# Optimization experiments

Hardware: AMD Instinct MI355X
Metric: run time of the kernel (lower is better)

The kernel has to match this reference:

```python
import jax, jax.numpy as jnp
import numpy as np

TAU = 0.5
EPS = 1e-6
RAY_STEPS = 128
N_SECANT = 8
STEPS_IN = 64
STEPS_OUT = 32
RADIUS = 1.0
ADA_START, ADA_END, ADA_DECAY = 2.0, 0.1, 1.5e-5
IT = 100000
DEPTH_NEAR = 0.0
DELTA = float(max(ADA_START * np.exp(-ADA_DECAY * IT), ADA_END))


def _occ_val(p, W1, b1, W2, b2):
    # occupancy probability minus tau (sign change = surface crossing)
    h = jax.nn.softplus(p @ W1 + b1)
    return jax.nn.sigmoid((h @ W2 + b2)[..., 0]) - TAU


def _rgb_alpha(p, v, W1, b1, W2, b2, Wc1, bc1, Wc2, bc2):
    alpha = _occ_val(p, W1, b1, W2, b2) + TAU
    f = jax.nn.relu(jnp.concatenate([p, v], -1) @ Wc1 + bc1)
    rgb = jax.nn.sigmoid(f @ Wc2 + bc2)
    return rgb, alpha


def _forward(pixels, camera_mat, world_mat, scale_mat, W1, b1, W2, b2, Wc1, bc1, Wc2, bc2):
    B, N, _ = pixels.shape
    # transform_to_world with all matrices inverted: p_world = S^-1 W^-1 C^-1 p_hom
    M = jnp.linalg.inv(scale_mat) @ jnp.linalg.inv(world_mat) @ jnp.linalg.inv(camera_mat)
    ones = jnp.ones((B, N, 1), pixels.dtype)
    p_h = jnp.concatenate([pixels, ones, ones], -1)  # (x, y, 1, 1) with depth 1
    pixels_world = jnp.einsum('bij,bnj->bni', M, p_h)[..., :3]
    origin = jnp.array([0.0, 0.0, 0.0, 1.0], pixels.dtype)
    cam0 = jnp.einsum('bij,j->bi', M, origin)[..., :3]                 # (B,3)
    camera_world = jnp.broadcast_to(cam0[:, None, :], (B, N, 3))
    ray = pixels_world - camera_world
    ray = ray / jnp.linalg.norm(ray, axis=-1, keepdims=True)

    # ---- sphere intersection ----
    rcd = jnp.einsum('bnd,bd->bn', ray, cam0)
    under = rcd ** 2 - (jnp.sum(cam0 ** 2, -1)[:, None] - RADIUS ** 2)
    mask_int = under > 0
    s = jnp.sqrt(jnp.where(mask_int, under, 1.0))                      # safe sqrt
    inters = jnp.stack([-s - rcd, s - rcd], -1)
    inters = jnp.where(mask_int[..., None], inters, 0.0)
    inters = jnp.maximum(inters, 0.0)                                  # (B,N,2)
    d_far = inters[..., 1]

    # ---- ray marching + secant root finding (no grad in original) ----
    t = jnp.linspace(0.0, 1.0, RAY_STEPS, dtype=pixels.dtype)
    d_prop = d_far[..., None] * t                                      # (B,N,S)
    p_prop = camera_world[:, :, None, :] + ray[:, :, None, :] * d_prop[..., None]
    val = _occ_val(p_prop, W1, b1, W2, b2)                             # (B,N,S)
    mask_0_free = val[..., 0] < 0
    sign = jnp.sign(val[..., :-1] * val[..., 1:])
    sign = jnp.concatenate([sign, jnp.ones_like(sign[..., :1])], -1)
    cost = sign * jnp.arange(RAY_STEPS, 0, -1, dtype=pixels.dtype)
    ind = jnp.argmin(cost, -1)
    mask_sc = jnp.min(cost, -1) < 0
    f_low = jnp.take_along_axis(val, ind[..., None], -1)[..., 0]
    mask = mask_sc & (f_low < 0) & mask_int & mask_0_free
    ind_hi = jnp.minimum(ind + 1, RAY_STEPS - 1)
    d_low = jnp.take_along_axis(d_prop, ind[..., None], -1)[..., 0]
    d_high = jnp.take_along_axis(d_prop, ind_hi[..., None], -1)[..., 0]
    f_high = jnp.take_along_axis(val, ind_hi[..., None], -1)[..., 0]

    def sec(f_l, f_h, d_l, d_h):
        den = f_h - f_l
        return jnp.where(jnp.abs(den) > 1e-12, -f_l * (d_h - d_l) / den + d_l, 0.5 * (d_l + d_h))

    def body(i, c):
        d_p, d_l, f_l, d_h, f_h = c
        f_m = _occ_val(camera_world + ray * d_p[..., None], W1, b1, W2, b2)
        low = f_m < 0
        d_l = jnp.where(low, d_p, d_l); f_l = jnp.where(low, f_m, f_l)
        d_h = jnp.where(low, d_h, d_p); f_h = jnp.where(low, f_h, f_m)
        return (sec(f_l, f_h, d_l, d_h), d_l, f_l, d_h, f_h)

    d_pred0 = sec(f_low, f_high, d_low, d_high)
    d_pred, _, _, _, _ = jax.lax.fori_loop(0, N_SECANT, body, (d_pred0, d_low, f_low, d_high, f_high))
    d_i = jnp.where(mask, d_pred, jnp.inf)
    d_i = jnp.where(mask_0_free, d_i, 0.0)
    d_i = jax.lax.stop_gradient(d_i)

    # ---- depth interval selection ----
    mask_zero = d_i == 0
    mask_pred = jnp.isfinite(d_i)
    dists = jnp.where(mask_pred, d_i, 1.0)
    dists = jnp.where(mask_zero, 0.0, dists)[0]                        # batch 1, as original
    obj_mask = (mask_pred & ~mask_zero)[0]                             # (N,)
    cam_f = camera_world.reshape(-1, 3)
    ray_f = ray.reshape(-1, 3)
    d_surf = inters.reshape(-1, 2)[:, 1]
    dnp = jnp.maximum(dists - DELTA, DEPTH_NEAR)
    dfp = jnp.minimum(dists + DELTA, d_surf)
    FULL = STEPS_IN + STEPS_OUT
    t_full = jnp.linspace(0.0, 1.0, FULL, dtype=pixels.dtype)
    d_bg = d_surf[:, None] * t_full                                    # depth_range[0] = 0
    t_in = jnp.linspace(0.0, 1.0, STEPS_IN, dtype=pixels.dtype)
    t_out = jnp.linspace(0.0, 1.0, STEPS_OUT, dtype=pixels.dtype)
    d_in = dnp[:, None] * (1.0 - t_in) + dfp[:, None] * t_in
    d_out = dnp[:, None] * t_out
    d_obj = jnp.sort(jnp.concatenate([d_out, d_in], -1), -1)
    d_all = jnp.where(obj_mask[:, None], d_obj, d_bg)                  # (N, FULL)

    # ---- shading + alpha compositing ----
    p_fg = cam_f[:, None, :] + ray_f[:, None, :] * d_all[..., None]    # (N,FULL,3)
    v_fg = jnp.broadcast_to(-ray_f[:, None, :], p_fg.shape)
    rgb, alpha = _rgb_alpha(p_fg, v_fg, W1, b1, W2, b2, Wc1, bc1, Wc2, bc2)
    trans = jnp.cumprod(jnp.concatenate([jnp.ones_like(alpha[:, :1]), 1.0 - alpha + EPS], -1), -1)[:, :-1]
    w = alpha * trans
    rgb_values = jnp.sum(w[..., None] * rgb, -2)
    return rgb_values.reshape(B, N, 3)


def setup_inputs() -> dict:
    key = jax.random.key(0)
    ks = jax.random.split(key, 8)
    B, N, H = 1, 4096, 128
    pixels = jax.random.uniform(ks[0], (B, N, 2), minval=-1.0, maxval=1.0, dtype=jnp.float32)
    camera_mat = jnp.broadcast_to(jnp.diag(jnp.array([2.0, 2.0, 1.0, 1.0], jnp.float32)), (B, 4, 4))
    world_mat = jnp.broadcast_to(jnp.array([[1, 0, 0, 0], [0, 1, 0, 0], [0, 0, 1, 2.0], [0, 0, 0, 1]], jnp.float32), (B, 4, 4))
    scale_mat = jnp.broadcast_to(jnp.eye(4, dtype=jnp.float32), (B, 4, 4))
    W1 = jax.random.normal(ks[1], (3, H), jnp.float32)
    b1 = 0.1 * jax.random.normal(ks[2], (H,), jnp.float32)
    W2 = 0.5 * jax.random.normal(ks[3], (H, 1), jnp.float32)
    b2 = jnp.zeros((1,), jnp.float32)
    Wc1 = 0.5 * jax.random.normal(ks[4], (6, H), jnp.float32)
    bc1 = jnp.zeros((H,), jnp.float32)
    Wc2 = 0.5 * jax.random.normal(ks[5], (H, 3), jnp.float32)
    bc2 = jnp.zeros((3,), jnp.float32)
    return dict(pixels=pixels, camera_mat=camera_mat, world_mat=world_mat, scale_mat=scale_mat,
                W1=W1, b1=b1, W2=W2, b2=b2, Wc1=Wc1, bc1=bc1, Wc2=Wc2, bc2=bc2)


def reference(pixels, camera_mat, world_mat, scale_mat, W1, b1, W2, b2, Wc1, bc1, Wc2, bc2):
    return _forward(pixels, camera_mat, world_mat, scale_mat, W1, b1, W2, b2, Wc1, bc1, Wc2, bc2)
```

## Files before the change

kernel.cpp:

```cpp
#include <hip/hip_runtime.h>
#include <math.h>


namespace {

constexpr int H_    = 128;
constexpr int RS    = 128;
constexpr int NSEC  = 8;
constexpr int SOUT_ = 32;
constexpr int SIN_  = 64;
constexpr int FULL_ = 96;
constexpr int RPB   = 4;
constexpr float EPSA   = 1e-6f;
constexpr float DELTA_ = 0.44626032029685964f;
constexpr float L2E    = 1.4426950408889634f;
constexpr float LN2    = 0.6931471805599453f;

typedef __attribute__((ext_vector_type(2))) float f2;

__device__ __forceinline__ f2 s2(float v) { return f2{v, v}; }

constexpr float PC0 =  0.5849625007211562f;
constexpr float PC1 =  0.4808983469629878f;
constexpr float PC2 = -0.0801497244938313f;
constexpr float PC3 =  0.0178110498875181f;
constexpr float PC4 = -0.0044527624718795f;
constexpr float PC5 =  0.0011873633258345f;
constexpr float PC6 = -0.0003298231460651f;

__device__ __forceinline__ f2 sp2p(f2 u) {
    f2 e;
    e.x = __builtin_amdgcn_exp2f(-fabsf(u.x));
    e.y = __builtin_amdgcn_exp2f(-fabsf(u.y));
    f2 t = e + e - 1.0f;
    f2 p = s2(PC6);
    p = __builtin_elementwise_fma(p, t, s2(PC5));
    p = __builtin_elementwise_fma(p, t, s2(PC4));
    p = __builtin_elementwise_fma(p, t, s2(PC3));
    p = __builtin_elementwise_fma(p, t, s2(PC2));
    p = __builtin_elementwise_fma(p, t, s2(PC1));
    p = __builtin_elementwise_fma(p, t, s2(PC0));
    return __builtin_elementwise_max(u, s2(0.0f)) + p;
}

__device__ __forceinline__ float sigmoid_fast(float x) {
    return __builtin_amdgcn_rcpf(1.0f + __expf(-x));
}
__device__ __forceinline__ float sgnf(float p) {
    return (p > 0.0f) ? 1.0f : ((p < 0.0f) ? -1.0f : 0.0f);
}
__device__ __forceinline__ float secant_step(float f_l, float f_h, float d_l, float d_h) {
    float den = f_h - f_l;
    if (fabsf(den) > 1e-12f) return -f_l * (d_h - d_l) / den + d_l;
    return 0.5f * (d_l + d_h);
}
__device__ __forceinline__ float2 ld2(const float* p) {
    return *reinterpret_cast<const float2*>(p);
}

__device__ void inv4(const float* m, float* o) {
    float inv[16];
    inv[0]  =  m[5]*m[10]*m[15] - m[5]*m[11]*m[14] - m[9]*m[6]*m[15] + m[9]*m[7]*m[14] + m[13]*m[6]*m[11] - m[13]*m[7]*m[10];
    inv[4]  = -m[4]*m[10]*m[15] + m[4]*m[11]*m[14] + m[8]*m[6]*m[15] - m[8]*m[7]*m[14] - m[12]*m[6]*m[11] + m[12]*m[7]*m[10];
    inv[8]  =  m[4]*m[9]*m[15]  - m[4]*m[11]*m[13] - m[8]*m[5]*m[15] + m[8]*m[7]*m[13] + m[12]*m[5]*m[11] - m[12]*m[7]*m[9];
    inv[12] = -m[4]*m[9]*m[14]  + m[4]*m[10]*m[13] + m[8]*m[5]*m[14] - m[8]*m[6]*m[13] - m[12]*m[5]*m[10] + m[12]*m[6]*m[9];
    inv[1]  = -m[1]*m[10]*m[15] + m[1]*m[11]*m[14] + m[9]*m[2]*m[15] - m[9]*m[3]*m[14] - m[13]*m[2]*m[11] + m[13]*m[3]*m[10];
    inv[5]  =  m[0]*m[10]*m[15] - m[0]*m[11]*m[14] - m[8]*m[2]*m[15] + m[8]*m[3]*m[14] + m[12]*m[2]*m[11] - m[12]*m[3]*m[10];
    inv[9]  = -m[0]*m[9]*m[15]  + m[0]*m[11]*m[13] + m[8]*m[1]*m[15] - m[8]*m[3]*m[13] - m[12]*m[1]*m[11] + m[12]*m[3]*m[9];
    inv[13] =  m[0]*m[9]*m[14]  - m[0]*m[10]*m[13] - m[8]*m[1]*m[14] + m[8]*m[2]*m[13] + m[12]*m[1]*m[10] - m[12]*m[2]*m[9];
    inv[2]  =  m[1]*m[6]*m[15]  - m[1]*m[7]*m[14]  - m[5]*m[2]*m[15] + m[5]*m[3]*m[14] + m[13]*m[2]*m[7]  - m[13]*m[3]*m[6];
    inv[6]  = -m[0]*m[6]*m[15]  + m[0]*m[7]*m[14]  + m[4]*m[2]*m[15] - m[4]*m[3]*m[14] - m[12]*m[2]*m[7]  + m[12]*m[3]*m[6];
    inv[10] =  m[0]*m[5]*m[15]  - m[0]*m[7]*m[13]  - m[4]*m[1]*m[15] + m[4]*m[3]*m[13] + m[12]*m[1]*m[7]  - m[12]*m[3]*m[5];
    inv[14] = -m[0]*m[5]*m[14]  + m[0]*m[6]*m[13]  + m[4]*m[1]*m[14] - m[4]*m[2]*m[13] - m[12]*m[1]*m[6]  + m[12]*m[2]*m[5];
    inv[3]  = -m[1]*m[6]*m[11]  + m[1]*m[7]*m[10]  + m[5]*m[2]*m[11] - m[5]*m[3]*m[10] - m[9]*m[2]*m[7]   + m[9]*m[3]*m[6];
    inv[7]  =  m[0]*m[6]*m[11]  - m[0]*m[7]*m[10]  - m[4]*m[2]*m[11] + m[4]*m[3]*m[10] + m[8]*m[2]*m[7]   - m[8]*m[3]*m[6];
    inv[11] = -m[0]*m[5]*m[11]  + m[0]*m[7]*m[9]   + m[4]*m[1]*m[11] - m[4]*m[3]*m[9]  - m[8]*m[1]*m[7]   + m[8]*m[3]*m[5];
    inv[15] =  m[0]*m[5]*m[10]  - m[0]*m[6]*m[9]   - m[4]*m[1]*m[10] + m[4]*m[2]*m[9]  + m[8]*m[1]*m[6]   - m[8]*m[2]*m[5];
    float det = m[0]*inv[0] + m[1]*inv[4] + m[2]*inv[8] + m[3]*inv[12];
    float idet = 1.0f / det;
    for (int i = 0; i < 16; i++) o[i] = inv[i] * idet;
}

__global__ __launch_bounds__(64 * RPB) void render_k(
    const float* __restrict__ pixels,
    const float* __restrict__ Cm, const float* __restrict__ Wm, const float* __restrict__ Sm,
    const float* __restrict__ W1, const float* __restrict__ b1,
    const float* __restrict__ W2, const float* __restrict__ b2,
    const float* __restrict__ Wc1, const float* __restrict__ bc1,
    const float* __restrict__ Wc2, const float* __restrict__ bc2,
    float* __restrict__ out, int N)
{
    const int tid  = threadIdx.x;
    const int lane = tid & 63;
    const int wid  = tid >> 6;
    const int r    = blockIdx.x * RPB + wid;
    const int rr   = (r < N) ? r : (N - 1);

    __shared__ float4 sP0[RPB][H_/2];
    __shared__ float4 sP1[RPB][H_/2];
    __shared__ float4 sP2[RPB][H_/2];
    __shared__ float4 sP3[RPB][H_/2];
    __shared__ f2     sW2[RPB][H_/2];
    __shared__ float  sInv[3][16];
    __shared__ float  sT[16], sM[16];

    const int u0 = 2 * lane;
    const float2 w1xv = ld2(W1 + u0);
    const float2 w1yv = ld2(W1 + H_ + u0);
    const float2 w1zv = ld2(W1 + 2*H_ + u0);
    const float2 b1v  = ld2(b1 + u0);
    const float2 w2v  = ld2(W2 + u0);
    const float2 q0v  = ld2(Wc1 + u0);
    const float2 q1v  = ld2(Wc1 + H_ + u0);
    const float2 q2v  = ld2(Wc1 + 2*H_ + u0);
    const float2 q3v  = ld2(Wc1 + 3*H_ + u0);
    const float2 q4v  = ld2(Wc1 + 4*H_ + u0);
    const float2 q5v  = ld2(Wc1 + 5*H_ + u0);
    const float2 bc1v = ld2(bc1 + u0);
    const float2 wc2a = ld2(Wc2 + 3*u0);
    const float2 wc2b = ld2(Wc2 + 3*u0 + 2);
    const float2 wc2c = ld2(Wc2 + 3*u0 + 4);
    const float b2v  = b2[0];
    const float bc20 = bc2[0], bc21 = bc2[1], bc22 = bc2[2];

    if (wid == 0) {
        const float* mm = (lane == 0) ? Cm : ((lane == 1) ? Wm : Sm);
        float o[16];
        inv4(mm, o);
        if (lane < 3)
            for (int k = 0; k < 16; k++) sInv[lane][k] = o[k];
    }
    __syncthreads();
    if (wid == 0 && lane < 16) {
        int row = lane >> 2, col = lane & 3;
        float s = 0.0f;
        for (int k = 0; k < 4; k++) s += sInv[1][row*4 + k] * sInv[0][k*4 + col];
        sT[lane] = s;
    }
    __syncthreads();
    if (wid == 0 && lane < 16) {
        int row = lane >> 2, col = lane & 3;
        float s = 0.0f;
        for (int k = 0; k < 4; k++) s += sInv[2][row*4 + k] * sT[k*4 + col];
        sM[lane] = s;
    }
    __syncthreads();

    float cx, cy, cz, rx, ry, rz, dfar;
    int mint;
    {
        const float px_ = pixels[2*rr], py_ = pixels[2*rr + 1];
        float cam[3], dir[3];
        for (int i = 0; i < 3; i++) {
            cam[i] = sM[4*i + 3];
            float pw = sM[4*i + 0]*px_ + sM[4*i + 1]*py_ + sM[4*i + 2] + sM[4*i + 3];
            dir[i] = pw - cam[i];
        }
        float nrm = sqrtf(dir[0]*dir[0] + dir[1]*dir[1] + dir[2]*dir[2]);
        rx = dir[0]/nrm; ry = dir[1]/nrm; rz = dir[2]/nrm;
        cx = cam[0]; cy = cam[1]; cz = cam[2];
        float rcd = rx*cx + ry*cy + rz*cz;
        float cc  = cx*cx + cy*cy + cz*cz;
        float under = rcd*rcd - (cc - 1.0f);
        mint = under > 0.0f;
        float s = sqrtf(mint ? under : 1.0f);
        dfar = mint ? fmaxf(s - rcd, 0.0f) : 0.0f;
    }

    float a2k[2], c2k[2], w2k[2];
    float cCr[2], w0r[2], w1r[2], w2r[2];
    {
        a2k[0] = (w1xv.x*rx + w1yv.x*ry + w1zv.x*rz) * L2E;
        a2k[1] = (w1xv.y*rx + w1yv.y*ry + w1zv.y*rz) * L2E;
        c2k[0] = (w1xv.x*cx + w1yv.x*cy + w1zv.x*cz + b1v.x) * L2E;
        c2k[1] = (w1xv.y*cx + w1yv.y*cy + w1zv.y*cz + b1v.y) * L2E;
        w2k[0] = w2v.x * LN2;
        w2k[1] = w2v.y * LN2;
        float aC0 = q0v.x*rx + q1v.x*ry + q2v.x*rz;
        float aC1 = q0v.y*rx + q1v.y*ry + q2v.y*rz;
        cCr[0] = q0v.x*cx + q1v.x*cy + q2v.x*cz + bc1v.x - (q3v.x*rx + q4v.x*ry + q5v.x*rz);
        cCr[1] = q0v.y*cx + q1v.y*cy + q2v.y*cz + bc1v.y - (q3v.y*rx + q4v.y*ry + q5v.y*rz);
        w0r[0] = wc2a.x; w1r[0] = wc2a.y; w2r[0] = wc2b.x;
        w0r[1] = wc2b.y; w1r[1] = wc2c.x; w2r[1] = wc2c.y;
        sP0[wid][lane] = float4{a2k[0], a2k[1], c2k[0], c2k[1]};
        sP1[wid][lane] = float4{w2k[0], w2k[1], aC0, aC1};
        sP2[wid][lane] = float4{cCr[0], cCr[1], w0r[0], w0r[1]};
        sP3[wid][lane] = float4{w1r[0], w1r[1], w2r[0], w2r[1]};
        sW2[wid][lane] = f2{w2k[0], w2k[1]};
    }
    __syncthreads();

    float alpha0, r0c, g0c, b0c;
    float alpha1, r1c, g1c, b1c;

    if (dfar == 0.0f) {
        f2 sp = sp2p(f2{c2k[0], c2k[1]});
        float part = sp.x*w2k[0] + sp.y*w2k[1];
        f2 ff = __builtin_elementwise_max(f2{cCr[0], cCr[1]}, s2(0.0f));
        float A0 = ff.x*w0r[0] + ff.y*w0r[1];
        float A1 = ff.x*w1r[0] + ff.y*w1r[1];
        float A2 = ff.x*w2r[0] + ff.y*w2r[1];
#pragma unroll
        for (int off = 32; off; off >>= 1) {
            part += __shfl_xor(part, off, 64);
            A0   += __shfl_xor(A0,   off, 64);
            A1   += __shfl_xor(A1,   off, 64);
            A2   += __shfl_xor(A2,   off, 64);
        }
        alpha0 = sigmoid_fast(part + b2v);
        r0c = sigmoid_fast(A0 + bc20);
        g0c = sigmoid_fast(A1 + bc21);
        b0c = sigmoid_fast(A2 + bc22);
        alpha1 = alpha0; r1c = r0c; g1c = g0c; b1c = b0c;
    } else {
        const float inv127 = 1.0f / (RS - 1);

        float l0;
        {
            f2 sp = sp2p(f2{c2k[0], c2k[1]});
            float part = sp.x*w2k[0] + sp.y*w2k[1];
#pragma unroll
            for (int off = 32; off; off >>= 1) part += __shfl_xor(part, off, 64);
            l0 = part + b2v;
        }

        float d_i;
        if (l0 >= 0.0f) {
            d_i = 0.0f;
        } else {
            auto march_logit = [&](float dsmp) -> float {
                const f2 dd = s2(dsmp);
                f2 acc = s2(0.0f);
#pragma unroll 4
                for (int j2 = 0; j2 < H_/2; j2++) {
                    float4 q0 = sP0[wid][j2];
                    f2 wv = sW2[wid][j2];
                    f2 u = __builtin_elementwise_fma(f2{q0.x, q0.y}, dd, f2{q0.z, q0.w});
                    acc = __builtin_elementwise_fma(sp2p(u), wv, acc);
                }
                return acc.x + acc.y + b2v;
            };

            float lA = march_logit(dfar * ((float)lane * inv127));
            float va = sigmoid_fast(lA) - 0.5f;
            float van = __shfl_down(va, 1, 64);
            float ca = (lane < 63) ? sgnf(va * van) * (float)(RS - lane) : 1.0f;
            float cmin = ca; int ind = lane;
#pragma unroll
            for (int off = 32; off; off >>= 1) {
                float c2 = __shfl_xor(cmin, off, 64);
                int   i2 = __shfl_xor(ind,  off, 64);
                if (c2 < cmin || (c2 == cmin && i2 < ind)) { cmin = c2; ind = i2; }
            }
            int crossed = cmin < 0.0f;
            float f_low = 0.0f, f_high = 0.0f;
            if (crossed) {
                f_low  = __shfl(va, ind, 64);
                f_high = __shfl(va, ind + 1, 64);
            } else {
                float lB = march_logit(dfar * ((float)(lane + 64) * inv127));
                float vb = sigmoid_fast(lB) - 0.5f;
                float v63 = __shfl(va, 63, 64);
                float v64 = __shfl(vb, 0, 64);
                if (v63 * v64 < 0.0f) {
                    crossed = 1; ind = 63;
                    f_low = v63; f_high = v64;
                } else {
                    float vbn = __shfl_down(vb, 1, 64);
                    float cb = (lane < 63) ? sgnf(vb * vbn) * (float)(64 - lane) : 1.0f;
                    float cminb = cb; int indl = lane;
#pragma unroll
                    for (int off = 32; off; off >>= 1) {
                        float c2 = __shfl_xor(cminb, off, 64);
                        int   i2 = __shfl_xor(indl,  off, 64);
                        if (c2 < cminb || (c2 == cminb && i2 < indl)) { cminb = c2; indl = i2; }
                    }
                    if (cminb < 0.0f) {
                        crossed = 1; ind = 64 + indl;
                        f_low  = __shfl(vb, indl, 64);
                        f_high = __shfl(vb, indl + 1, 64);
                    }
                }
            }

            const int msk = crossed && (f_low < 0.0f) && mint;
            if (msk) {
                float d_l = dfar * ((float)ind * inv127);
                float d_h = dfar * ((float)(ind + 1) * inv127);
                float f_l = f_low, f_h = f_high;
                float d_p = secant_step(f_l, f_h, d_l, d_h);
                for (int it = 0; it < NSEC; it++) {
                    f2 u2 = __builtin_elementwise_fma(f2{a2k[0], a2k[1]}, s2(d_p),
                                                      f2{c2k[0], c2k[1]});
                    f2 sp = sp2p(u2);
                    float part = sp.x*w2k[0] + sp.y*w2k[1];
#pragma unroll
                    for (int off = 32; off; off >>= 1) part += __shfl_xor(part, off, 64);
                    float fm = sigmoid_fast(part + b2v) - 0.5f;
                    bool low = fm < 0.0f;
                    d_l = low ? d_p : d_l;  f_l = low ? fm : f_l;
                    d_h = low ? d_h : d_p;  f_h = low ? f_h : fm;
                    d_p = secant_step(f_l, f_h, d_l, d_h);
                }
                d_i = d_p;
            } else {
                d_i = INFINITY;
            }
        }

        const int mask_zero = (d_i == 0.0f);
        const int mask_pred = isfinite(d_i);
        float dists = mask_pred ? d_i : 1.0f;
        if (mask_zero) dists = 0.0f;
        const int obj = mask_pred && !mask_zero;
        const float dnp = fmaxf(dists - DELTA_, 0.0f);
        const float dfp = fminf(dists + DELTA_, dfar);

        auto sample_d = [&](int s) -> float {
            if (obj) {
                if (s < SOUT_) return dnp * ((float)s * (1.0f / (SOUT_ - 1)));
                float u = (float)(s - SOUT_) * (1.0f / (SIN_ - 1));
                return dnp * (1.0f - u) + dfp * u;
            }
            return dfar * ((float)s * (1.0f / (FULL_ - 1)));
        };

        {
            const f2 dd = s2(sample_d(lane));
            f2 SO = s2(0.0f), A0 = s2(0.0f), A1 = s2(0.0f), A2 = s2(0.0f);
#pragma unroll 4
            for (int j2 = 0; j2 < H_/2; j2++) {
                float4 q0 = sP0[wid][j2];
                float4 q1 = sP1[wid][j2];
                float4 q2 = sP2[wid][j2];
                float4 q3 = sP3[wid][j2];
                f2 u = __builtin_elementwise_fma(f2{q0.x, q0.y}, dd, f2{q0.z, q0.w});
                SO = __builtin_elementwise_fma(sp2p(u), f2{q1.x, q1.y}, SO);
                f2 f = __builtin_elementwise_max(
                           __builtin_elementwise_fma(f2{q1.z, q1.w}, dd, f2{q2.x, q2.y}),
                           s2(0.0f));
                A0 = __builtin_elementwise_fma(f, f2{q2.z, q2.w}, A0);
                A1 = __builtin_elementwise_fma(f, f2{q3.x, q3.y}, A1);
                A2 = __builtin_elementwise_fma(f, f2{q3.z, q3.w}, A2);
            }
            alpha0 = sigmoid_fast(SO.x + SO.y + b2v);
            r0c = sigmoid_fast(A0.x + A0.y + bc20);
            g0c = sigmoid_fast(A1.x + A1.y + bc21);
            b0c = sigmoid_fast(A2.x + A2.y + bc22);
        }

        {
            const int s1 = 64 + (lane & 31);
            const int jb = (lane >> 5) * (H_/4);
            const f2 dd = s2(sample_d(s1));
            f2 SO = s2(0.0f), A0 = s2(0.0f), A1 = s2(0.0f), A2 = s2(0.0f);
#pragma unroll 4
            for (int j2 = jb; j2 < jb + H_/4; j2++) {
                float4 q0 = sP0[wid][j2];
                float4 q1 = sP1[wid][j2];
                float4 q2 = sP2[wid][j2];
                float4 q3 = sP3[wid][j2];
                f2 u = __builtin_elementwise_fma(f2{q0.x, q0.y}, dd, f2{q0.z, q0.w});
                SO = __builtin_elementwise_fma(sp2p(u), f2{q1.x, q1.y}, SO);
                f2 f = __builtin_elementwise_max(
                           __builtin_elementwise_fma(f2{q1.z, q1.w}, dd, f2{q2.x, q2.y}),
                           s2(0.0f));
                A0 = __builtin_elementwise_fma(f, f2{q2.z, q2.w}, A0);
                A1 = __builtin_elementwise_fma(f, f2{q3.x, q3.y}, A1);
                A2 = __builtin_elementwise_fma(f, f2{q3.z, q3.w}, A2);
            }
            float SOs = SO.x + SO.y, A0s = A0.x + A0.y;
            float A1s = A1.x + A1.y, A2s = A2.x + A2.y;
            SOs += __shfl_xor(SOs, 32, 64);
            A0s += __shfl_xor(A0s, 32, 64);
            A1s += __shfl_xor(A1s, 32, 64);
            A2s += __shfl_xor(A2s, 32, 64);
            alpha1 = sigmoid_fast(SOs + b2v);
            r1c = sigmoid_fast(A0s + bc20);
            g1c = sigmoid_fast(A1s + bc21);
            b1c = sigmoid_fast(A2s + bc22);
        }
    }

    {
        float mA = 1.0f - alpha0 + EPSA;
        float p = mA;
#pragma unroll
        for (int off = 1; off < 64; off <<= 1) {
            float v = __shfl_up(p, off, 64);
            if (lane >= off) p *= v;
        }
        float TexA = __shfl_up(p, 1, 64);
        if (lane == 0) TexA = 1.0f;
        float TA = __shfl(p, 63, 64);
        float wA = alpha0 * TexA;

        float mB = (lane < 32) ? (1.0f - alpha1 + EPSA) : 1.0f;
        float pb = mB;
#pragma unroll
        for (int off = 1; off < 32; off <<= 1) {
            float v = __shfl_up(pb, off, 64);
            if (lane >= off) pb *= v;
        }
        float TexB = __shfl_up(pb, 1, 64);
        if (lane == 0) TexB = 1.0f;
        float wB = (lane < 32) ? alpha1 * TexB * TA : 0.0f;

        float s0 = wA*r0c + wB*r1c;
        float s1 = wA*g0c + wB*g1c;
        float s2v = wA*b0c + wB*b1c;
#pragma unroll
        for (int off = 32; off; off >>= 1) {
            s0  += __shfl_xor(s0,  off, 64);
            s1  += __shfl_xor(s1,  off, 64);
            s2v += __shfl_xor(s2v, off, 64);
        }
        if (lane == 0 && r < N) {
            out[3*r + 0] = s0;
            out[3*r + 1] = s1;
            out[3*r + 2] = s2v;
        }
    }
}

}

extern "C" void kernel_launch(void* const* d_in, const int* in_sizes, int n_in,
                              void* d_out, int out_size, void* d_ws, size_t ws_size,
                              hipStream_t stream) {
    const float* pixels = (const float*)d_in[0];
    const float* Cm  = (const float*)d_in[1];
    const float* Wm  = (const float*)d_in[2];
    const float* Sm  = (const float*)d_in[3];
    const float* W1  = (const float*)d_in[4];
    const float* b1  = (const float*)d_in[5];
    const float* W2  = (const float*)d_in[6];
    const float* b2  = (const float*)d_in[7];
    const float* Wc1 = (const float*)d_in[8];
    const float* bc1 = (const float*)d_in[9];
    const float* Wc2 = (const float*)d_in[10];
    const float* bc2 = (const float*)d_in[11];
    float* out = (float*)d_out;

    const int N = in_sizes[0] / 2;
    const int nblk = (N + RPB - 1) / RPB;
    hipLaunchKernelGGL(render_k, dim3(nblk), dim3(64 * RPB), 0, stream,
                       pixels, Cm, Wm, Sm, W1, b1, W2, b2, Wc1, bc1, Wc2, bc2, out, N);
}
```

Before: 98.98 us.

## Split each ray's hidden dimension across two waves and use Estrin polynomial

Each block now handles one ray with two wavefronts, each covering half of the 128 hidden units. Partial logits and colour sums are exchanged through shared memory with block barriers, and the compositing scan is split between the two waves. The intent is to halve per-wave serial work per ray and raise parallelism. The cost is extra __syncthreads and shared-memory traffic. The softplus polynomial is also evaluated in Estrin form to shorten its dependency chain.

```diff
diff --git a/kernel.cpp b/kernel.cpp
--- a/kernel.cpp
+++ b/kernel.cpp
@@ -10,7 +10,6 @@
 constexpr int SOUT_ = 32;
 constexpr int SIN_  = 64;
 constexpr int FULL_ = 96;
-constexpr int RPB   = 4;
 constexpr float EPSA   = 1e-6f;
 constexpr float DELTA_ = 0.44626032029685964f;
 constexpr float L2E    = 1.4426950408889634f;
@@ -32,14 +31,15 @@
     f2 e;
     e.x = __builtin_amdgcn_exp2f(-fabsf(u.x));
     e.y = __builtin_amdgcn_exp2f(-fabsf(u.y));
-    f2 t = e + e - 1.0f;
-    f2 p = s2(PC6);
-    p = __builtin_elementwise_fma(p, t, s2(PC5));
-    p = __builtin_elementwise_fma(p, t, s2(PC4));
-    p = __builtin_elementwise_fma(p, t, s2(PC3));
-    p = __builtin_elementwise_fma(p, t, s2(PC2));
-    p = __builtin_elementwise_fma(p, t, s2(PC1));
-    p = __builtin_elementwise_fma(p, t, s2(PC0));
+    f2 t  = e + e - 1.0f;
+    f2 t2 = t * t;
+    f2 t4 = t2 * t2;
+    f2 A = __builtin_elementwise_fma(t, s2(PC1), s2(PC0));
+    f2 B = __builtin_elementwise_fma(t, s2(PC3), s2(PC2));
+    f2 C = __builtin_elementwise_fma(t, s2(PC5), s2(PC4));
+    f2 E = __builtin_elementwise_fma(t2, B, A);
+    f2 F = __builtin_elementwise_fma(t2, s2(PC6), C);
+    f2 p = __builtin_elementwise_fma(t4, F, E);
     return __builtin_elementwise_max(u, s2(0.0f)) + p;
 }
 
@@ -81,7 +81,7 @@
     for (int i = 0; i < 16; i++) o[i] = inv[i] * idet;
 }
 
-__global__ __launch_bounds__(64 * RPB) void render_k(
+__global__ __launch_bounds__(128, 8) void render_k(
     const float* __restrict__ pixels,
     const float* __restrict__ Cm, const float* __restrict__ Wm, const float* __restrict__ Sm,
     const float* __restrict__ W1, const float* __restrict__ b1,
@@ -93,16 +93,21 @@
     const int tid  = threadIdx.x;
     const int lane = tid & 63;
     const int wid  = tid >> 6;
-    const int r    = blockIdx.x * RPB + wid;
-    const int rr   = (r < N) ? r : (N - 1);
-
-    __shared__ float4 sP0[RPB][H_/2];
-    __shared__ float4 sP1[RPB][H_/2];
-    __shared__ float4 sP2[RPB][H_/2];
-    __shared__ float4 sP3[RPB][H_/2];
-    __shared__ f2     sW2[RPB][H_/2];
+    const int r    = blockIdx.x;
+    const int base = wid * 32;
+
+    __shared__ float4 sP0[H_/2];
+    __shared__ float4 sP1[H_/2];
+    __shared__ float4 sP2[H_/2];
+    __shared__ float4 sP3[H_/2];
+    __shared__ f2     sW2[H_/2];
     __shared__ float  sInv[3][16];
     __shared__ float  sT[16], sM[16];
+    __shared__ float  sLgA[2][64];
+    __shared__ float  sLgB[2][64];
+    __shared__ float4 sEx0[2][64];
+    __shared__ float4 sEx1[2][32];
+    __shared__ float  sCmp[4];
 
     const int u0 = 2 * lane;
     const float2 w1xv = ld2(W1 + u0);
@@ -110,16 +115,19 @@
     const float2 w1zv = ld2(W1 + 2*H_ + u0);
     const float2 b1v  = ld2(b1 + u0);
     const float2 w2v  = ld2(W2 + u0);
-    const float2 q0v  = ld2(Wc1 + u0);
-    const float2 q1v  = ld2(Wc1 + H_ + u0);
-    const float2 q2v  = ld2(Wc1 + 2*H_ + u0);
-    const float2 q3v  = ld2(Wc1 + 3*H_ + u0);
-    const float2 q4v  = ld2(Wc1 + 4*H_ + u0);
-    const float2 q5v  = ld2(Wc1 + 5*H_ + u0);
-    const float2 bc1v = ld2(bc1 + u0);
-    const float2 wc2a = ld2(Wc2 + 3*u0);
-    const float2 wc2b = ld2(Wc2 + 3*u0 + 2);
-    const float2 wc2c = ld2(Wc2 + 3*u0 + 4);
+    float2 q0v{}, q1v{}, q2v{}, q3v{}, q4v{}, q5v{}, bc1v{}, wc2a{}, wc2b{}, wc2c{};
+    if (wid == 0) {
+        q0v  = ld2(Wc1 + u0);
+        q1v  = ld2(Wc1 + H_ + u0);
+        q2v  = ld2(Wc1 + 2*H_ + u0);
+        q3v  = ld2(Wc1 + 3*H_ + u0);
+        q4v  = ld2(Wc1 + 4*H_ + u0);
+        q5v  = ld2(Wc1 + 5*H_ + u0);
+        bc1v = ld2(bc1 + u0);
+        wc2a = ld2(Wc2 + 3*u0);
+        wc2b = ld2(Wc2 + 3*u0 + 2);
+        wc2c = ld2(Wc2 + 3*u0 + 4);
+    }
     const float b2v  = b2[0];
     const float bc20 = bc2[0], bc21 = bc2[1], bc22 = bc2[2];
 
@@ -149,7 +157,7 @@
     float cx, cy, cz, rx, ry, rz, dfar;
     int mint;
     {
-        const float px_ = pixels[2*rr], py_ = pixels[2*rr + 1];
+        const float px_ = pixels[2*r], py_ = pixels[2*r + 1];
         float cam[3], dir[3];
         for (int i = 0; i < 3; i++) {
             cam[i] = sM[4*i + 3];
@@ -168,7 +176,6 @@
     }
 
     float a2k[2], c2k[2], w2k[2];
-    float cCr[2], w0r[2], w1r[2], w2r[2];
     {
         a2k[0] = (w1xv.x*rx + w1yv.x*ry + w1zv.x*rz) * L2E;
         a2k[1] = (w1xv.y*rx + w1yv.y*ry + w1zv.y*rz) * L2E;
@@ -176,30 +183,32 @@
         c2k[1] = (w1xv.y*cx + w1yv.y*cy + w1zv.y*cz + b1v.y) * L2E;
         w2k[0] = w2v.x * LN2;
         w2k[1] = w2v.y * LN2;
-        float aC0 = q0v.x*rx + q1v.x*ry + q2v.x*rz;
-        float aC1 = q0v.y*rx + q1v.y*ry + q2v.y*rz;
-        cCr[0] = q0v.x*cx + q1v.x*cy + q2v.x*cz + bc1v.x - (q3v.x*rx + q4v.x*ry + q5v.x*rz);
-        cCr[1] = q0v.y*cx + q1v.y*cy + q2v.y*cz + bc1v.y - (q3v.y*rx + q4v.y*ry + q5v.y*rz);
-        w0r[0] = wc2a.x; w1r[0] = wc2a.y; w2r[0] = wc2b.x;
-        w0r[1] = wc2b.y; w1r[1] = wc2c.x; w2r[1] = wc2c.y;
-        sP0[wid][lane] = float4{a2k[0], a2k[1], c2k[0], c2k[1]};
-        sP1[wid][lane] = float4{w2k[0], w2k[1], aC0, aC1};
-        sP2[wid][lane] = float4{cCr[0], cCr[1], w0r[0], w0r[1]};
-        sP3[wid][lane] = float4{w1r[0], w1r[1], w2r[0], w2r[1]};
-        sW2[wid][lane] = f2{w2k[0], w2k[1]};
+        if (wid == 0) {
+            float aC0 = q0v.x*rx + q1v.x*ry + q2v.x*rz;
+            float aC1 = q0v.y*rx + q1v.y*ry + q2v.y*rz;
+            float cC0 = q0v.x*cx + q1v.x*cy + q2v.x*cz + bc1v.x - (q3v.x*rx + q4v.x*ry + q5v.x*rz);
+            float cC1 = q0v.y*cx + q1v.y*cy + q2v.y*cz + bc1v.y - (q3v.y*rx + q4v.y*ry + q5v.y*rz);
+            sP0[lane] = float4{a2k[0], a2k[1], c2k[0], c2k[1]};
+            sP1[lane] = float4{w2k[0], w2k[1], aC0, aC1};
+            sP2[lane] = float4{cC0, cC1, wc2a.x, wc2b.y};
+            sP3[lane] = float4{wc2a.y, wc2c.x, wc2b.x, wc2c.y};
+            sW2[lane] = f2{w2k[0], w2k[1]};
+        }
     }
     __syncthreads();
 
-    float alpha0, r0c, g0c, b0c;
-    float alpha1, r1c, g1c, b1c;
+    float alpha0 = 0.0f, r0c = 0.0f, g0c = 0.0f, b0c = 0.0f;
+    float alpha1 = 0.0f, r1c = 0.0f, g1c = 0.0f, b1c = 0.0f;
 
     if (dfar == 0.0f) {
         f2 sp = sp2p(f2{c2k[0], c2k[1]});
         float part = sp.x*w2k[0] + sp.y*w2k[1];
-        f2 ff = __builtin_elementwise_max(f2{cCr[0], cCr[1]}, s2(0.0f));
-        float A0 = ff.x*w0r[0] + ff.y*w0r[1];
-        float A1 = ff.x*w1r[0] + ff.y*w1r[1];
-        float A2 = ff.x*w2r[0] + ff.y*w2r[1];
+        float4 p2 = sP2[lane];
+        float4 p3 = sP3[lane];
+        f2 ff = __builtin_elementwise_max(f2{p2.x, p2.y}, s2(0.0f));
+        float A0 = ff.x*p2.z + ff.y*p2.w;
+        float A1 = ff.x*p3.x + ff.y*p3.y;
+        float A2 = ff.x*p3.z + ff.y*p3.w;
 #pragma unroll
         for (int off = 32; off; off >>= 1) {
             part += __shfl_xor(part, off, 64);
@@ -228,23 +237,24 @@
         if (l0 >= 0.0f) {
             d_i = 0.0f;
         } else {
-            auto march_logit = [&](float dsmp) -> float {
+            auto march32 = [&](float dsmp) -> float {
                 const f2 dd = s2(dsmp);
                 f2 acc = s2(0.0f);
 #pragma unroll 4
-                for (int j2 = 0; j2 < H_/2; j2++) {
-                    float4 q0 = sP0[wid][j2];
-                    f2 wv = sW2[wid][j2];
+                for (int j = 0; j < 32; ++j) {
+                    float4 q0 = sP0[base + j];
+                    f2 wv = sW2[base + j];
                     f2 u = __builtin_elementwise_fma(f2{q0.x, q0.y}, dd, f2{q0.z, q0.w});
                     acc = __builtin_elementwise_fma(sp2p(u), wv, acc);
                 }
-                return acc.x + acc.y + b2v;
+                return acc.x + acc.y;
             };
 
-            float lA = march_logit(dfar * ((float)lane * inv127));
-            float va = sigmoid_fast(lA) - 0.5f;
-            float van = __shfl_down(va, 1, 64);
-            float ca = (lane < 63) ? sgnf(va * van) * (float)(RS - lane) : 1.0f;
+            sLgA[wid][lane] = march32(dfar * ((float)lane * inv127));
+            __syncthreads();
+            float va = (sLgA[0][lane] + sLgA[1][lane]) + b2v;
+            float lan = __shfl_down(va, 1, 64);
+            float ca = (lane < 63) ? sgnf(va * lan) * (float)(RS - lane) : 1.0f;
             float cmin = ca; int ind = lane;
 #pragma unroll
             for (int off = 32; off; off >>= 1) {
@@ -253,21 +263,22 @@
                 if (c2 < cmin || (c2 == cmin && i2 < ind)) { cmin = c2; ind = i2; }
             }
             int crossed = cmin < 0.0f;
-            float f_low = 0.0f, f_high = 0.0f;
+            float ll = 0.0f, lh = 0.0f;
             if (crossed) {
-                f_low  = __shfl(va, ind, 64);
-                f_high = __shfl(va, ind + 1, 64);
+                ll = __shfl(va, ind, 64);
+                lh = __shfl(va, ind + 1, 64);
             } else {
-                float lB = march_logit(dfar * ((float)(lane + 64) * inv127));
-                float vb = sigmoid_fast(lB) - 0.5f;
-                float v63 = __shfl(va, 63, 64);
-                float v64 = __shfl(vb, 0, 64);
-                if (v63 * v64 < 0.0f) {
+                sLgB[wid][lane] = march32(dfar * ((float)(lane + 64) * inv127));
+                __syncthreads();
+                float vb = (sLgB[0][lane] + sLgB[1][lane]) + b2v;
+                float l63 = __shfl(va, 63, 64);
+                float l64 = __shfl(vb, 0, 64);
+                if (l63 * l64 < 0.0f) {
                     crossed = 1; ind = 63;
-                    f_low = v63; f_high = v64;
+                    ll = l63; lh = l64;
                 } else {
-                    float vbn = __shfl_down(vb, 1, 64);
-                    float cb = (lane < 63) ? sgnf(vb * vbn) * (float)(64 - lane) : 1.0f;
+                    float lbn = __shfl_down(vb, 1, 64);
+                    float cb = (lane < 63) ? sgnf(vb * lbn) * (float)(64 - lane) : 1.0f;
                     float cminb = cb; int indl = lane;
 #pragma unroll
                     for (int off = 32; off; off >>= 1) {
@@ -277,17 +288,18 @@
                     }
                     if (cminb < 0.0f) {
                         crossed = 1; ind = 64 + indl;
-                        f_low  = __shfl(vb, indl, 64);
-                        f_high = __shfl(vb, indl + 1, 64);
+                        ll = __shfl(vb, indl, 64);
+                        lh = __shfl(vb, indl + 1, 64);
                     }
                 }
             }
 
-            const int msk = crossed && (f_low < 0.0f) && mint;
+            const int msk = crossed && (ll < 0.0f) && mint;
             if (msk) {
+                float f_l = sigmoid_fast(ll) - 0.5f;
+                float f_h = sigmoid_fast(lh) - 0.5f;
                 float d_l = dfar * ((float)ind * inv127);
                 float d_h = dfar * ((float)(ind + 1) * inv127);
-                float f_l = f_low, f_h = f_high;
                 float d_p = secant_step(f_l, f_h, d_l, d_h);
                 for (int it = 0; it < NSEC; it++) {
                     f2 u2 = __builtin_elementwise_fma(f2{a2k[0], a2k[1]}, s2(d_p),
@@ -329,11 +341,11 @@
             const f2 dd = s2(sample_d(lane));
             f2 SO = s2(0.0f), A0 = s2(0.0f), A1 = s2(0.0f), A2 = s2(0.0f);
 #pragma unroll 4
-            for (int j2 = 0; j2 < H_/2; j2++) {
-                float4 q0 = sP0[wid][j2];
-                float4 q1 = sP1[wid][j2];
-                float4 q2 = sP2[wid][j2];
-                float4 q3 = sP3[wid][j2];
+            for (int j = 0; j < 32; ++j) {
+                float4 q0 = sP0[base + j];
+                float4 q1 = sP1[base + j];
+                float4 q2 = sP2[base + j];
+                float4 q3 = sP3[base + j];
                 f2 u = __builtin_elementwise_fma(f2{q0.x, q0.y}, dd, f2{q0.z, q0.w});
                 SO = __builtin_elementwise_fma(sp2p(u), f2{q1.x, q1.y}, SO);
                 f2 f = __builtin_elementwise_max(
@@ -343,23 +355,19 @@
                 A1 = __builtin_elementwise_fma(f, f2{q3.x, q3.y}, A1);
                 A2 = __builtin_elementwise_fma(f, f2{q3.z, q3.w}, A2);
             }
-            alpha0 = sigmoid_fast(SO.x + SO.y + b2v);
-            r0c = sigmoid_fast(A0.x + A0.y + bc20);
-            g0c = sigmoid_fast(A1.x + A1.y + bc21);
-            b0c = sigmoid_fast(A2.x + A2.y + bc22);
-        }
-
+            sEx0[wid][lane] = float4{SO.x + SO.y, A0.x + A0.y, A1.x + A1.y, A2.x + A2.y};
+        }
         {
             const int s1 = 64 + (lane & 31);
-            const int jb = (lane >> 5) * (H_/4);
+            const int jb = base + (lane >> 5) * 16;
             const f2 dd = s2(sample_d(s1));
             f2 SO = s2(0.0f), A0 = s2(0.0f), A1 = s2(0.0f), A2 = s2(0.0f);
 #pragma unroll 4
-            for (int j2 = jb; j2 < jb + H_/4; j2++) {
-                float4 q0 = sP0[wid][j2];
-                float4 q1 = sP1[wid][j2];
-                float4 q2 = sP2[wid][j2];
-                float4 q3 = sP3[wid][j2];
+            for (int j = jb; j < jb + 16; ++j) {
+                float4 q0 = sP0[j];
+                float4 q1 = sP1[j];
+                float4 q2 = sP2[j];
+                float4 q3 = sP3[j];
                 f2 u = __builtin_elementwise_fma(f2{q0.x, q0.y}, dd, f2{q0.z, q0.w});
                 SO = __builtin_elementwise_fma(sp2p(u), f2{q1.x, q1.y}, SO);
                 f2 f = __builtin_elementwise_max(
@@ -375,16 +383,27 @@
             A0s += __shfl_xor(A0s, 32, 64);
             A1s += __shfl_xor(A1s, 32, 64);
             A2s += __shfl_xor(A2s, 32, 64);
-            alpha1 = sigmoid_fast(SOs + b2v);
-            r1c = sigmoid_fast(A0s + bc20);
-            g1c = sigmoid_fast(A1s + bc21);
-            b1c = sigmoid_fast(A2s + bc22);
-        }
-    }
-
-    {
-        float mA = 1.0f - alpha0 + EPSA;
-        float p = mA;
+            if (lane < 32) sEx1[wid][lane] = float4{SOs, A0s, A1s, A2s};
+        }
+        __syncthreads();
+
+        if (wid == 0) {
+            float4 a = sEx0[0][lane], b = sEx0[1][lane];
+            alpha0 = sigmoid_fast(a.x + b.x + b2v);
+            r0c = sigmoid_fast(a.y + b.y + bc20);
+            g0c = sigmoid_fast(a.z + b.z + bc21);
+            b0c = sigmoid_fast(a.w + b.w + bc22);
+        } else {
+            float4 a = sEx1[0][lane & 31], b = sEx1[1][lane & 31];
+            alpha1 = sigmoid_fast(a.x + b.x + b2v);
+            r1c = sigmoid_fast(a.y + b.y + bc20);
+            g1c = sigmoid_fast(a.z + b.z + bc21);
+            b1c = sigmoid_fast(a.w + b.w + bc22);
+        }
+    }
+
+    if (wid == 0) {
+        float p = 1.0f - alpha0 + EPSA;
 #pragma unroll
         for (int off = 1; off < 64; off <<= 1) {
             float v = __shfl_up(p, off, 64);
@@ -394,31 +413,40 @@
         if (lane == 0) TexA = 1.0f;
         float TA = __shfl(p, 63, 64);
         float wA = alpha0 * TexA;
-
-        float mB = (lane < 32) ? (1.0f - alpha1 + EPSA) : 1.0f;
-        float pb = mB;
-#pragma unroll
-        for (int off = 1; off < 32; off <<= 1) {
-            float v = __shfl_up(pb, off, 64);
-            if (lane >= off) pb *= v;
-        }
-        float TexB = __shfl_up(pb, 1, 64);
-        if (lane == 0) TexB = 1.0f;
-        float wB = (lane < 32) ? alpha1 * TexB * TA : 0.0f;
-
-        float s0 = wA*r0c + wB*r1c;
-        float s1 = wA*g0c + wB*g1c;
-        float s2v = wA*b0c + wB*b1c;
+        float s0 = wA * r0c, s1 = wA * g0c, s2v = wA * b0c;
 #pragma unroll
         for (int off = 32; off; off >>= 1) {
             s0  += __shfl_xor(s0,  off, 64);
             s1  += __shfl_xor(s1,  off, 64);
             s2v += __shfl_xor(s2v, off, 64);
         }
-        if (lane == 0 && r < N) {
-            out[3*r + 0] = s0;
-            out[3*r + 1] = s1;
-            out[3*r + 2] = s2v;
+        if (lane == 0) {
+            sCmp[0] = TA; sCmp[1] = s0; sCmp[2] = s1; sCmp[3] = s2v;
+        }
+    }
+    __syncthreads();
+    if (wid == 1) {
+        const float TA = sCmp[0];
+        float pb = (lane < 32) ? (1.0f - alpha1 + EPSA) : 1.0f;
+#pragma unroll
+        for (int off = 1; off < 32; off <<= 1) {
+            float v = __shfl_up(pb, off, 64);
+            if (lane >= off) pb *= v;
+        }
+        float TexB = __shfl_up(pb, 1, 64);
+        if (lane == 0) TexB = 1.0f;
+        float wB = (lane < 32) ? alpha1 * TexB * TA : 0.0f;
+        float t0 = wB * r1c, t1 = wB * g1c, t2 = wB * b1c;
+#pragma unroll
+        for (int off = 32; off; off >>= 1) {
+            t0 += __shfl_xor(t0, off, 64);
+            t1 += __shfl_xor(t1, off, 64);
+            t2 += __shfl_xor(t2, off, 64);
+        }
+        if (lane == 0) {
+            out[3*r + 0] = sCmp[1] + t0;
+            out[3*r + 1] = sCmp[2] + t1;
+            out[3*r + 2] = sCmp[3] + t2;
         }
     }
 }
@@ -443,7 +471,6 @@
     float* out = (float*)d_out;
 
     const int N = in_sizes[0] / 2;
-    const int nblk = (N + RPB - 1) / RPB;
-    hipLaunchKernelGGL(render_k, dim3(nblk), dim3(64 * RPB), 0, stream,
+    hipLaunchKernelGGL(render_k, dim3(N), dim3(128), 0, stream,
                        pixels, Cm, Wm, Sm, W1, b1, W2, b2, Wc1, bc1, Wc2, bc2, out, N);
 }
```

New measurement: 111.1 us. +12.3%, slower.
